# Kernel optimization log

Measured on AMD Instinct MI355X. Metric: run time of the kernel, lower is better.

Reference implementation:

```python
import jax, jax.numpy as jnp
import numpy as np

# BatchNorm1d in eval mode with default init (gamma=1, beta=0, mean=0, var=1):
# y = x / sqrt(1 + eps)
BN_S = 1.0 / float(np.sqrt(1.0 + 1e-5))
ROI_THRESH = 0.8
DN = ('NCHW', 'OIHW', 'NCHW')


def conv(x, w, stride=1, pad=1):
    return jax.lax.conv_general_dilated(x, w, (stride, stride), ((pad, pad), (pad, pad)), dimension_numbers=DN)


def inv_conv(x, w):
    # dense equivalent of spconv.SparseInverseConv2d paired with a stride-2, pad-1, k=3 conv:
    # adjoint index map = transposed conv (lhs_dilation=2, flipped kernel, pad (1,2))
    return jax.lax.conv_general_dilated(x, jnp.flip(w, (2, 3)), (1, 1), ((1, 2), (1, 2)), lhs_dilation=(2, 2), dimension_numbers=DN)


def downsample_mask(m):
    # active-site generation rule of a stride-2, pad-1, k=3 sparse conv == 3x3/stride-2 max pool
    return jax.lax.reduce_window(m, 0.0, jax.lax.max, (1, 1, 3, 3), (1, 1, 2, 2), ((0, 0), (0, 0), (1, 1), (1, 1)))


def setup_inputs():
    key = jax.random.key(0)
    ks = jax.random.split(key, 24)
    b, n_i, H, W = 2, 4, 384, 384
    s = 0.1  # weight scale to keep activations bounded through the conv stack
    inp = {
        'x': jax.random.normal(ks[0], (b, 64, H // 4, W // 4), jnp.float32),
        'image': jax.random.normal(ks[1], (b, 3, H, W), jnp.float32),
        'masks': jax.random.uniform(ks[2], (b, n_i, H, W), jnp.float32),
        'roi_masks': jax.random.uniform(ks[3], (b, n_i, H, W), jnp.float32),
        'w1a': jax.random.normal(ks[4], (32, 4, 3, 3), jnp.float32) * s,
        'w1b': jax.random.normal(ks[5], (32, 32, 3, 3), jnp.float32) * s,
        'w2a': jax.random.normal(ks[6], (32, 32, 3, 3), jnp.float32) * s,
        'w2b': jax.random.normal(ks[7], (32, 32, 3, 3), jnp.float32) * s,
        'w4a': jax.random.normal(ks[8], (64, 32, 3, 3), jnp.float32) * s,
        'w4b': jax.random.normal(ks[9], (64, 64, 3, 3), jnp.float32) * s,
        'inv4_w': jax.random.normal(ks[10], (64, 64, 3, 3), jnp.float32) * s,
        'l4_sub_w': jax.random.normal(ks[11], (32, 64, 3, 3), jnp.float32) * s,
        'inv2_w': jax.random.normal(ks[12], (32, 32, 3, 3), jnp.float32) * s,
        'l5_sub_w': jax.random.normal(ks[13], (32, 32, 3, 3), jnp.float32) * s,
        'r4_w1': jax.random.normal(ks[14], (32, 64, 3, 3), jnp.float32) * s,
        'r4_w2': jax.random.normal(ks[15], (1, 32, 3, 3), jnp.float32) * s,
        'r4_b2': jax.random.normal(ks[16], (1,), jnp.float32) * s,
        'r1_w1': jax.random.normal(ks[17], (32, 32, 3, 3), jnp.float32) * s,
        'r1_w2': jax.random.normal(ks[18], (1, 32, 3, 3), jnp.float32) * s,
        'r1_b2': jax.random.normal(ks[19], (1,), jnp.float32) * s,
    }
    return inp


def reference(x, image, masks, roi_masks, w1a, w1b, w2a, w2b, w4a, w4b, inv4_w, l4_sub_w, inv2_w, l5_sub_w, r4_w1, r4_w2, r4_b2, r1_w1, r1_w2, r1_b2):
    # Faithful dense emulation of predict_details: SubMConv == conv(masked x)*mask,
    # stride-2 SparseConv == conv(masked x) masked by max-pooled mask,
    # SparseInverseConv == transposed conv masked by parent-resolution mask,
    # Fsp.sparse_add on shared indices == masked add, dense()-99/+99 == where(mask, v, -99).
    b, n_i, H, W = masks.shape
    N = b * n_i
    m = masks.reshape(N, 1, H, W)
    roi = roi_masks.reshape(N, 1, H, W)
    img = jnp.broadcast_to(image[:, None], (b, n_i, 3, H, W)).reshape(N, 3, H, W)
    inp = jnp.concatenate([img, m], axis=1)  # [N,4,H,W]

    mask1 = (roi > ROI_THRESH).astype(inp.dtype)
    mask2 = downsample_mask(mask1)
    mask4 = downsample_mask(mask2)

    # low_os1_module: SubMConv, ReLU, BN, SubMConv, ReLU, BN
    f = jnp.maximum(conv(inp * mask1, w1a) * mask1, 0.0) * BN_S
    fea1 = jnp.maximum(conv(f, w1b) * mask1, 0.0) * BN_S  # [N,32,H,W]
    # low_os2_module: stride-2 SparseConv, ReLU, BN, SubMConv, ReLU, BN
    g = jnp.maximum(conv(fea1, w2a, stride=2) * mask2, 0.0) * BN_S
    fea2 = jnp.maximum(conv(g, w2b) * mask2, 0.0) * BN_S  # [N,32,H/2,W/2]
    # low_os4_module
    h = jnp.maximum(conv(fea2, w4a, stride=2) * mask4, 0.0) * BN_S
    fea3 = jnp.maximum(conv(h, w4b) * mask4, 0.0) * BN_S  # [N,64,H/4,W/4]

    # gather dense OS4 features at sparse sites (batch index // n_i) + sparse_add
    xg = jnp.broadcast_to(x[:, None], (b, n_i) + x.shape[1:]).reshape(N, *x.shape[1:]) * mask4
    xs = xg + fea3

    # refine_OS4: SubMConv, BN, leaky, SubMConv(+bias); dense() with -99 off-support
    t = jax.nn.leaky_relu(conv(xs, r4_w1) * mask4 * BN_S, 0.2)
    t = (conv(t, r4_w2) + r4_b2[None, :, None, None]) * mask4
    x_os4_out = jnp.where(mask4 > 0, t, -99.0)

    # layer4: SparseInverseConv(64->64) to OS2 sites, BN, leaky, SubMConv(64->32); add fea2
    u = jax.nn.leaky_relu(inv_conv(xs, inv4_w) * mask2 * BN_S, 0.2)
    u = conv(u, l4_sub_w) * mask2 + fea2
    # layer5: SparseInverseConv(32->32) to OS1 sites, BN, leaky, SubMConv(32->32); add fea1
    v = jax.nn.leaky_relu(inv_conv(u, inv2_w) * mask1 * BN_S, 0.2)
    v = conv(v, l5_sub_w) * mask1 + fea1

    # refine_OS1
    t1 = jax.nn.leaky_relu(conv(v, r1_w1) * mask1 * BN_S, 0.2)
    t1 = (conv(t1, r1_w2) + r1_b2[None, :, None, None]) * mask1
    x_os1_out = jnp.where(mask1 > 0, t1, -99.0)
    return x_os4_out, x_os1_out
```

## Files before the change

kernel.cpp:

```cpp
#include <hip/hip_runtime.h>
#include <hip/hip_bf16.h>

using bf16 = __hip_bfloat16;
typedef unsigned char u8;
typedef short bf16x8 __attribute__((ext_vector_type(8)));
typedef short bf16x4 __attribute__((ext_vector_type(4)));
typedef float f32x4 __attribute__((ext_vector_type(4)));

#define BNS 0.9999950000374997f
#define MFMA_B16 __builtin_amdgcn_mfma_f32_16x16x32_bf16

__device__ __forceinline__ short f2bs(float v){ bf16 h = __float2bfloat16(v); return *reinterpret_cast<short*>(&h); }
__device__ __forceinline__ float s2f(short s){ union{unsigned u; float f;} x; x.u = ((unsigned)(unsigned short)s) << 16; return x.f; }
__device__ __forceinline__ float lrelu(float a){ return fmaxf(a, 0.2f*a); }
__device__ __forceinline__ bf16x8 ld8(const short* p){ return *(const bf16x8*)(p); }


__global__ __launch_bounds__(256) void k_mask1(const float* __restrict__ roi, u8* __restrict__ m1, int total){
    int i = blockIdx.x*256 + threadIdx.x;
    if (i < total) m1[i] = (roi[i] > 0.8f) ? 1 : 0;
}

__global__ __launch_bounds__(256) void k_down(const u8* __restrict__ mi, u8* __restrict__ mo,
                                              int IH, int IW, int OH, int OW){
    int p = blockIdx.x*256 + threadIdx.x;
    int n = blockIdx.y;
    if (p >= OH*OW) return;
    int oy = p / OW, ox = p - oy*OW;
    const u8* src = mi + (size_t)n*IH*IW;
    int v = 0;
    #pragma unroll
    for (int ky=0; ky<3; ky++){
        int iy = 2*oy + ky - 1;
        if ((unsigned)iy >= (unsigned)IH) continue;
        #pragma unroll
        for (int kx=0; kx<3; kx++){
            int ix = 2*ox + kx - 1;
            if ((unsigned)ix < (unsigned)IW) v |= src[iy*IW + ix];
        }
    }
    mo[(size_t)n*OH*OW + p] = (u8)v;
}

__global__ __launch_bounds__(256) void k_wprep(const float* __restrict__ w1b,
                                               const float* __restrict__ i2,
                                               const float* __restrict__ l5,
                                               const float* __restrict__ r1a,
                                               const float* __restrict__ w2b,
                                               const float* __restrict__ w2a,
                                               short* __restrict__ dst){
    int a = blockIdx.y;
    const float* src = (a==0)? w1b : (a==1)? i2 : (a==2)? l5 : (a==3)? r1a : (a==4)? w2b : w2a;
    float sc = (a==2) ? 1.0f : BNS;
    int j = blockIdx.x*256 + threadIdx.x;
    if (j < 9216){
        int co = j/288, r = j%288, ci = r/9, k = r%9;
        dst[a*9216 + k*1024 + co*32 + ci] = f2bs(src[j]*sc);
    }
}

__global__ __launch_bounds__(256) void k_wprep4(const float* __restrict__ inv4,
                                                const float* __restrict__ w4b,
                                                const float* __restrict__ l4s,
                                                const float* __restrict__ r4w1,
                                                const float* __restrict__ w4a,
                                                short* __restrict__ dst)
{
    int a = blockIdx.y;
// ... 87 lines not shown
        for (int g=0; g<G; ++g) acc[u2][g] = (f32x4){0,0,0,0};

    #pragma unroll
    for (int h=0; h<HV; ++h){
        const short* bh[U2N];
        #pragma unroll
        for (int u2=0; u2<U2N; ++u2){
            int ty = u2*4 + wv;
            bh[u2] = s_in + (h*4+nQ)*PS + (ty*18 + nn)*8;
        }
        #pragma unroll
        for (int ky=0; ky<3; ++ky)
            #pragma unroll
            for (int kx=0; kx<3; ++kx){
                const int k = ky*3+kx;
                bf16x8 a[G];
                #pragma unroll
                for (int g=0; g<G; ++g)
                    a[g] = *(const bf16x8*)(wT + k*COUT*CIN + (g*16+nn)*CIN + h*32 + nQ*8);
                #pragma unroll
                for (int u2=0; u2<U2N; ++u2){
                    bf16x8 bfr = ld8(bh[u2] + (ky*18+kx)*8);
                    #pragma unroll
                    for (int g=0; g<G; ++g)
                        acc[u2][g] = MFMA_B16(a[g], bfr, acc[u2][g], 0,0,0);
                }
            }
    }

    #pragma unroll
    for (int u2=0; u2<U2N; ++u2){
        int nt = u2*4 + wv;
        int p = (y0+nt)*H + x0+nn;
        u8 m = s_m[nt*16 + nn];
        short* op = out + ((size_t)n*HW + p)*COUT;
        #pragma unroll
        for (int g=0; g<G; ++g){
            float r[4];
            #pragma unroll
            for (int e=0; e<4; ++e){
                int co = g*16 + nQ*4 + e;
                float a = acc[u2][g][e], o;
                if      (EPI == 0) o = m ? fmaxf(a,0.f) : 0.f;
                else if (EPI == 1) o = m ? lrelu(a) : 0.f;
                else o = m ? fmaxf(a,0.f) + res32[((size_t)(n>>2)*COUT + co)*(size_t)HW + p] : 0.f;
                r[e] = o;
            }
            bf16x4 w4 = {f2bs(r[0]),f2bs(r[1]),f2bs(r[2]),f2bs(r[3])};
            *(bf16x4*)(op + g*16 + nQ*4) = w4;
        }
    }
}

template<int TH>
__global__ __launch_bounds__(256) void mconv_head32(const short* __restrict__ in, int H,
                                                    const short* __restrict__ wTh,
                                                    const float* __restrict__ bias,
                                                    const u8* __restrict__ mask,
                                                    float* __restrict__ out, int tilesX)
{
    const int HW = H*H;
    const int SR = TH + 2, SITES = SR*18;
    const int PS = (SITES|1)*8;
    int tY = blockIdx.x / tilesX, tX = blockIdx.x % tilesX, n = blockIdx.z;
    int y0 = tY*TH, x0 = tX*16;

    __shared__ __align__(16) short s_in[4*((SITES|1)*8)];
    __shared__ u8 s_m[TH*16];

    int tid = threadIdx.x;
    const short* inN = in + (size_t)n*HW*32;
    for (int i = tid; i < SITES*4; i += 256){
        int r = i>>2, q = i&3;
        int ry = r/18, rx = r%18;
        int gy = y0-1+ry, gx = x0-1+rx;
        bf16x8 v = {0,0,0,0,0,0,0,0};
        if ((unsigned)gy < (unsigned)H && (unsigned)gx < (unsigned)H)
            v = *(const bf16x8*)(inN + ((size_t)gy*H + gx)*32 + q*8);
        *(bf16x8*)(s_in + q*PS + r*8) = v;
    }
    for (int i = tid; i < TH*16; i += 256){
        int ty = i>>4, tx = i&15;
        s_m[i] = mask[(size_t)n*HW + (y0+ty)*H + x0+tx];
    }
    __syncthreads();

    int wv = tid >> 6, lane = tid & 63;
    int nQ = lane >> 4, nn = lane & 15;
    float bb = bias[0];

    for (int nt = wv; nt < TH; nt += 4){
        const short* bp = s_in + nQ*PS + (nt*18 + nn)*8;
        f32x4 acc = {0,0,0,0};
        #pragma unroll
        for (int ky=0; ky<3; ++ky)
            #pragma unroll
            for (int kx=0; kx<3; ++kx){
                const int k = ky*3+kx;
                bf16x8 aw = *(const bf16x8*)(wTh + k*512 + nn*32 + nQ*8);
                bf16x8 bfr = ld8(bp + (ky*18+kx)*8);
                acc = MFMA_B16(aw, bfr, acc, 0,0,0);
            }
        if (nQ == 0){
            u8 m = s_m[nt*16 + nn];
            int p = (y0+nt)*H + x0+nn;
            out[(size_t)n*HW + p] = m ? acc[0] + bb : -99.f;
        }
    }
}

template<int COUT, int THO>
__global__ __launch_bounds__(256) void mconv_s2m(const short* __restrict__ in, int IH,
                                                 const short* __restrict__ wT,
                                                 const u8* __restrict__ mask,
                                                 short* __restrict__ out, int OH, int tilesX)
{
    const int IHW = IH*IH, OHW = OH*OH, G = COUT/16;
    const int IR = 2*THO + 1;
    const int SITES = IR*33;
    const int PS = (SITES|1)*8;
    const int ITN = THO/4;
    int tY = blockIdx.x / tilesX, tX = blockIdx.x % tilesX, n = blockIdx.z;
    int y0 = tY*THO, x0 = tX*16;

    __shared__ __align__(16) short s_in[4*((SITES|1)*8)];
    __shared__ u8 s_m[THO*16];

    int tid = threadIdx.x;
    const short* inN = in + (size_t)n*IHW*32;
    for (int i = tid; i < SITES*4; i += 256){
        int r = i>>2, q = i&3;
        int ry = r/33, rx = r%33;
        int gy = 2*y0-1+ry, gx = 2*x0-1+rx;
        bf16x8 v = {0,0,0,0,0,0,0,0};
        if ((unsigned)gy < (unsigned)IH && (unsigned)gx < (unsigned)IH)
            v = *(const bf16x8*)(inN + ((size_t)gy*IH + gx)*32 + q*8);
        *(bf16x8*)(s_in + q*PS + r*8) = v;
    }
    for (int i = tid; i < THO*16; i += 256){
        int ty = i>>4, tx = i&15;
        s_m[i] = mask[(size_t)n*OHW + (y0+ty)*OH + x0+tx];
    }
    __syncthreads();

    int wv = tid >> 6, lane = tid & 63;
    int nQ = lane >> 4, nn = lane & 15;

    f32x4 acc[ITN][G];
    #pragma unroll
    for (int it=0; it<ITN; ++it)
        #pragma unroll
        for (int g=0; g<G; ++g) acc[it][g] = (f32x4){0,0,0,0};

    const short* pb[ITN];
    #pragma unroll
    for (int it=0; it<ITN; ++it){
        int nt = it*4 + wv;
        pb[it] = s_in + nQ*PS + ((2*nt)*33 + 2*nn)*8;
    }

    #pragma unroll
    for (int ky=0; ky<3; ++ky)
        #pragma unroll
        for (int kx=0; kx<3; ++kx){
            const int k = ky*3+kx;
            bf16x8 a[G];
            #pragma unroll
            for (int g=0; g<G; ++g)
                a[g] = *(const bf16x8*)(wT + k*COUT*32 + (g*16+nn)*32 + nQ*8);
            #pragma unroll
            for (int it=0; it<ITN; ++it){
                bf16x8 bfr = ld8(pb[it] + (ky*33+kx)*8);
                #pragma unroll
                for (int g=0; g<G; ++g)
                    acc[it][g] = MFMA_B16(a[g], bfr, acc[it][g], 0,0,0);
            }
        }

    #pragma unroll
    for (int it=0; it<ITN; ++it){
        int nt = it*4 + wv;
        int p = (y0+nt)*OH + x0+nn;
        u8 m = s_m[nt*16 + nn];
        short* op = out + ((size_t)n*OHW + p)*COUT;
        #pragma unroll
        for (int g=0; g<G; ++g){
            float r[4];
            #pragma unroll
            for (int e=0; e<4; ++e) r[e] = m ? fmaxf(acc[it][g][e],0.f) : 0.f;
            bf16x4 w4 = {f2bs(r[0]),f2bs(r[1]),f2bs(r[2]),f2bs(r[3])};
            *(bf16x4*)(op + g*16 + nQ*4) = w4;
        }
    }
}

__global__ __launch_bounds__(256) void conv1ab3(const float* __restrict__ image,
                                                const float* __restrict__ masks,
                                                const u8*  __restrict__ M1,
                                                const short* __restrict__ wT1a,
                                                const short* __restrict__ wT1b,
                                                short* __restrict__ fea1)
{
    const int H = 384; const int HW = H*H;
    const int PS = 181*8;
    int tY = blockIdx.x / 48, tX = blockIdx.x % 48, n = blockIdx.z;
    int y0 = tY*16, x0 = tX*8;

    __shared__ float s_inp[4][240];
    __shared__ u8    s_m[240];
    __shared__ int   s_cnt[2];
    __shared__ unsigned short s_lF[180];
    __shared__ unsigned short s_lO[128];
    __shared__ __align__(16) short s_ic[8*(181*8)];
    __shared__ __align__(16) short s_f[4*(181*8)];

    int tid = threadIdx.x;
    const bf16x8 Z8 = {0,0,0,0,0,0,0,0};
    if (tid < 2) s_cnt[tid] = 0;
    for (int i = tid; i < 4*181; i += 256)
        *(bf16x8*)(s_f + i*8) = Z8;
    for (int i = tid; i < 240; i += 256){
        int ly = i/12, lxx = i%12;
        int gy = y0-2+ly, gx = x0-2+lxx;
        bool inb = ((unsigned)gy < 384u) && ((unsigned)gx < 384u);
        u8 mv = inb ? M1[(size_t)n*HW + gy*H + gx] : 0;
        s_m[i] = mv;
        float mm = (float)mv;
        int p = gy*H + gx;
        #pragma unroll
        for (int c = 0; c < 4; ++c){
            float v = 0.f;
            if (inb) v = (c < 3) ? image[((size_t)(n>>2)*3 + c)*HW + p]
                                 : masks[(size_t)n*HW + p];
            s_inp[c][i] = v*mm;
        }
    }
    __syncthreads();

    for (int i = tid; i < 180; i += 256){
        int fy = i/10, fx = i - fy*10;
        if (s_m[(fy+1)*12 + fx+1]){
            int idx = atomicAdd(&s_cnt[0], 1);
            s_lF[idx] = (unsigned short)i;
        }
    }
    for (int i = tid; i < 128; i += 256){
        int ty = i>>3, tx = i&7;
        if (s_m[(ty+2)*12 + tx+2]){
            int idx = atomicAdd(&s_cnt[1], 1);
            s_lO[idx] = (unsigned short)i;
        }
    }
    __syncthreads();

    int cntF = s_cnt[0], cntO = s_cnt[1];

    {
        int q = tid & 63;
        int ci = q/9, kk = q - ci*9, ky = kk/3, kx = kk - ky*3;
        bool qok = q < 36;
        for (int i = tid; i < cntF*64; i += 256){
            int site = s_lF[i >> 6];
            short v = 0;
            if (qok){
                int fy = site/10, fx = site - fy*10;
                v = f2bs(s_inp[ci][(fy+ky)*12 + fx+kx]);
            }
            s_ic[(q>>3)*PS + site*8 + (q&7)] = v;
        }
    }
    __syncthreads();

    int wv = tid >> 6, lane = tid & 63;
    int nQ = lane >> 4, nn = lane & 15;

    {
        bf16x8 fa0[2], fa1[2];
        #pragma unroll
        for (int h=0;h<2;++h){
            fa0[h] = *(const bf16x8*)(wT1a + h*1024 + nn*32 + nQ*8);
            fa1[h] = *(const bf16x8*)(wT1a + h*1024 + (16+nn)*32 + nQ*8);
        }
        for (int base = wv*16; base < cntF; base += 64){
            int slot = base + nn;
            bool on = slot < cntF;
            int site = s_lF[on ? slot : 0];
            f32x4 a0 = {0,0,0,0}, a1 = {0,0,0,0};
            #pragma unroll
            for (int h=0;h<2;++h){
                bf16x8 bfr = ld8(s_ic + (h*4+nQ)*PS + site*8);
                a0 = MFMA_B16(fa0[h], bfr, a0, 0,0,0);
                a1 = MFMA_B16(fa1[h], bfr, a1, 0,0,0);
            }
            if (on){
                #pragma unroll
                for (int g=0; g<2; ++g){
                    float r[4];
                    #pragma unroll
                    for (int e=0; e<4; ++e){
                        float a = g ? a1[e] : a0[e];
                        r[e] = fmaxf(a,0.f);
                    }
                    bf16x4 w4 = {f2bs(r[0]),f2bs(r[1]),f2bs(r[2]),f2bs(r[3])};
                    *(bf16x4*)(s_f + (g*2 + (nQ>>1))*PS + site*8 + (nQ&1)*4) = w4;
                }
            }
        }
    }
    __syncthreads();

    {
        for (int base = wv*16; base < cntO; base += 64){
            int slot = base + nn;
            bool on = slot < cntO;
            int os = s_lO[on ? slot : 0];
            int ty = os >> 3, tx = os & 7;
            const short* pb = s_f + nQ*PS + (ty*10 + tx)*8;
            f32x4 acc0 = {0,0,0,0}, acc1 = {0,0,0,0};
            #pragma unroll
            for (int ky=0; ky<3; ++ky)
                #pragma unroll
                for (int kx=0; kx<3; ++kx){
                    const int k = ky*3+kx;
                    bf16x8 a0 = *(const bf16x8*)(wT1b + k*1024 + nn*32 + nQ*8);
                    bf16x8 a1 = *(const bf16x8*)(wT1b + k*1024 + (16+nn)*32 + nQ*8);
                    bf16x8 bfr = ld8(pb + (ky*10+kx)*8);
                    acc0 = MFMA_B16(a0, bfr, acc0, 0,0,0);
                    acc1 = MFMA_B16(a1, bfr, acc1, 0,0,0);
                }
// ... 163 lines not shown
                }
            }
        #pragma unroll
        for (int u2 = 0; u2 < 4; ++u2){
            int nt = u2*4 + wv;
            int p = (y0+nt)*H2 + x0+nn;
            u8 m = s_m[(nt+1)*18 + nn+1];
            short* up = u_out + ((size_t)n*HW2 + p)*32;
            #pragma unroll
            for (int g=0; g<2; ++g){
                float r[4];
                #pragma unroll
                for (int e=0; e<4; ++e){
                    float a = g ? acc1[u2][e] : acc0[u2][e];
                    r[e] = m ? a + s2f(pf2v[u2][g][e]) : 0.f;
                }
                bf16x4 w4 = {f2bs(r[0]),f2bs(r[1]),f2bs(r[2]),f2bs(r[3])};
                *(bf16x4*)(up + g*16 + nQ*4) = w4;
            }
        }
    }
}

__global__ __launch_bounds__(256) void fk_back8(const short* __restrict__ u,
                                                const short* __restrict__ fea1,
                                                const u8*  __restrict__ M1,
                                                const short* __restrict__ wTi2,
                                                const short* __restrict__ wTl5,
                                                const short* __restrict__ wTr1a,
                                                const short* __restrict__ wTr1b,
                                                const float* __restrict__ r1_b2,
                                                float* __restrict__ out1)
{
    const int H1 = 384, HW1 = H1*H1, H2 = 192, HW2 = H2*H2;
    const int PS_U = 97*8, PS_A = 309*8, PS_B = 241*8, PS_C = 181*8;
    int tY = blockIdx.x / 48, tX = blockIdx.x % 48, n = blockIdx.z;
    int y0 = tY*16, x0 = tX*8;
    int uy0 = (y0>>1) - 2, ux0 = (x0>>1) - 2;

    __shared__ __align__(16) short sP0[4*(309*8)];
    __shared__ __align__(16) short sP1[4*(241*8)];
    __shared__ u8 s_m[308];
    __shared__ int s_cnt[7];
    __shared__ unsigned s_lA[4*80];
    __shared__ unsigned s_lB[240];
    __shared__ unsigned s_lC[180];
    __shared__ unsigned s_lD[128];
    short* s_u  = sP1;
    short* s_vl = sP0;
    short* s_v  = sP1;
    short* s_t1 = sP0;

    int tid = threadIdx.x;
    const bf16x8 Z8 = {0,0,0,0,0,0,0,0};

    if (tid < 7) s_cnt[tid] = 0;
    const short* uN = u + (size_t)n*HW2*32;
    for (int i = tid; i < 96*4; i += 256){
        int r = i>>2, q = i&3;
        int ly = r >> 3, lxx = r & 7;
        int gy = uy0+ly, gx = ux0+lxx;
        bf16x8 v = Z8;
        if ((unsigned)gy < 192u && (unsigned)gx < 192u)
            v = *(const bf16x8*)(uN + ((size_t)gy*H2 + gx)*32 + q*8);
        *(bf16x8*)(s_u + q*PS_U + r*8) = v;
    }
    for (int i = tid; i < 308; i += 256){
        int ry = i/14, rx = i%14; int gy = y0-3+ry, gx = x0-3+rx;
        s_m[i] = ((unsigned)gy < 384u && (unsigned)gx < 384u) ? M1[(size_t)n*HW1 + gy*H1 + gx] : 0;
    }
    for (int i = tid; i < 4*309; i += 256)
        *(bf16x8*)(s_vl + i*8) = Z8;
    __syncthreads();

    for (int i = tid; i < 308; i += 256){
        if (s_m[i]){
            int ry = i/14, rx = i - ry*14;
            int cls = ((ry&1)<<1) | (rx&1);
            int jr = ry>>1, jc = rx>>1;
            int idx = atomicAdd(&s_cnt[cls], 1);
            s_lA[cls*80 + idx] = ((unsigned)i<<16) | (unsigned)(jr*8+jc);
        }
    }
    for (int i = tid; i < 240; i += 256){
        int vy = i/12, vx = i - vy*12;
        if (s_m[(vy+1)*14 + vx+1]){
            int idx = atomicAdd(&s_cnt[4], 1);
            s_lB[idx] = ((unsigned)i<<16) | (unsigned)(vy*14+vx);
        }
    }
    for (int i = tid; i < 180; i += 256){
        int qy = i/10, qx = i - qy*10;
        if (s_m[(qy+2)*14 + qx+2]){
            int idx = atomicAdd(&s_cnt[5], 1);
            s_lC[idx] = ((unsigned)i<<16) | (unsigned)(qy*12+qx);
        }
    }
    for (int i = tid; i < 128; i += 256){
        int ty = i>>3, tx = i&7;
        if (s_m[(ty+3)*14 + tx+3]){
            int idx = atomicAdd(&s_cnt[6], 1);
            s_lD[idx] = ((unsigned)i<<16) | (unsigned)(ty*10+tx);
        } else {
            out1[(size_t)n*HW1 + (size_t)(y0+ty)*H1 + (x0+tx)] = -99.f;
        }
    }
    __syncthreads();

    int wv = tid >> 6, lane = tid & 63;
    int nQ = lane >> 4, nn = lane & 15;

    {
        const int tN_[4]   = {4,2,2,1};
        const int tOff[4][4] = {{0,1,8,9},{1,9,9,9},{8,9,9,9},{9,9,9,9}};
        const int tWk [4][4] = {{8,6,2,0},{7,1,1,1},{5,3,3,3},{4,4,4,4}};
        int cnt = s_cnt[wv];
        int tn = tN_[wv];
        for (int base = 0; base < cnt; base += 16){
            int slot = base + nn;
            bool on = slot < cnt;
            unsigned e = s_lA[wv*80 + (on ? slot : 0)];
            int rb = e & 0xffff;
            f32x4 acc0 = {0,0,0,0}, acc1 = {0,0,0,0};
            for (int t = 0; t < tn; ++t){
                bf16x8 bfr = ld8(s_u + nQ*PS_U + (rb + tOff[wv][t])*8);
                const short* wp = wTi2 + tWk[wv][t]*1024;
                bf16x8 a0 = *(const bf16x8*)(wp + nn*32 + nQ*8);
                bf16x8 a1 = *(const bf16x8*)(wp + (16+nn)*32 + nQ*8);
                acc0 = MFMA_B16(a0, bfr, acc0, 0,0,0);
                acc1 = MFMA_B16(a1, bfr, acc1, 0,0,0);
            }
            if (on){
                int sidx = e >> 16;
                float r[8];
                #pragma unroll
                for (int g=0; g<2; ++g)
                    #pragma unroll
                    for (int ee=0; ee<4; ++ee)
                        r[g*4+ee] = lrelu(g ? acc1[ee] : acc0[ee]);
                bf16x4 w0 = {f2bs(r[0]),f2bs(r[1]),f2bs(r[2]),f2bs(r[3])};
                bf16x4 w1 = {f2bs(r[4]),f2bs(r[5]),f2bs(r[6]),f2bs(r[7])};
                *(bf16x4*)(s_vl + (nQ>>1)*PS_A     + sidx*8 + (nQ&1)*4) = w0;
                *(bf16x4*)(s_vl + (2+(nQ>>1))*PS_A + sidx*8 + (nQ&1)*4) = w1;
            }
        }
    }
    __syncthreads();

    for (int i = tid; i < 4*241; i += 256)
        *(bf16x8*)(s_v + i*8) = Z8;
    __syncthreads();

    {
        int cnt = s_cnt[4];
        for (int base = wv*16; base < cnt; base += 64){
            int slot = base + nn;
            bool on = slot < cnt;
            unsigned e = s_lB[on ? slot : 0];
            int rb = e & 0xffff;
            int wr = e >> 16;
            int vy = wr/12, vx = wr - vy*12;
            const short* f1 = fea1 + ((size_t)n*HW1 + (size_t)(y0-2+vy)*H1 + (x0-2+vx))*32;
            bf16x4 p0 = *(const bf16x4*)(f1 + nQ*4);
            bf16x4 p1 = *(const bf16x4*)(f1 + 16 + nQ*4);
            const short* pv = s_vl + nQ*PS_A + rb*8;
            f32x4 acc0 = {0,0,0,0}, acc1 = {0,0,0,0};
            #pragma unroll
            for (int ky=0; ky<3; ++ky)
                #pragma unroll
                for (int kx=0; kx<3; ++kx){
                    const int k = ky*3+kx;
                    bf16x8 wb0 = *(const bf16x8*)(wTl5 + k*1024 + nn*32 + nQ*8);
                    bf16x8 wb1 = *(const bf16x8*)(wTl5 + k*1024 + (16+nn)*32 + nQ*8);
                    bf16x8 bfr = ld8(pv + (ky*14+kx)*8);
                    acc0 = MFMA_B16(wb0, bfr, acc0, 0,0,0);
                    acc1 = MFMA_B16(wb1, bfr, acc1, 0,0,0);
                }
            if (on){
                float r[8];
                #pragma unroll
                for (int ee=0; ee<4; ++ee){
                    r[ee]   = acc0[ee] + s2f(p0[ee]);
                    r[4+ee] = acc1[ee] + s2f(p1[ee]);
                }
                bf16x4 w0 = {f2bs(r[0]),f2bs(r[1]),f2bs(r[2]),f2bs(r[3])};
                bf16x4 w1 = {f2bs(r[4]),f2bs(r[5]),f2bs(r[6]),f2bs(r[7])};
                *(bf16x4*)(s_v + (nQ>>1)*PS_B     + wr*8 + (nQ&1)*4) = w0;
                *(bf16x4*)(s_v + (2+(nQ>>1))*PS_B + wr*8 + (nQ&1)*4) = w1;
            }
        }
    }
    __syncthreads();

    for (int i = tid; i < 4*181; i += 256)
        *(bf16x8*)(s_t1 + i*8) = Z8;
    __syncthreads();

    {
        int cnt = s_cnt[5];
        for (int base = wv*16; base < cnt; base += 64){
            int slot = base + nn;
            bool on = slot < cnt;
            unsigned e = s_lC[on ? slot : 0];
            int rb = e & 0xffff;
            const short* pv = s_v + nQ*PS_B + rb*8;
            f32x4 acc0 = {0,0,0,0}, acc1 = {0,0,0,0};
            #pragma unroll
            for (int ky=0; ky<3; ++ky)
                #pragma unroll
                for (int kx=0; kx<3; ++kx){
                    const int k = ky*3+kx;
                    bf16x8 wc0 = *(const bf16x8*)(wTr1a + k*1024 + nn*32 + nQ*8);
                    bf16x8 wc1 = *(const bf16x8*)(wTr1a + k*1024 + (16+nn)*32 + nQ*8);
                    bf16x8 bfr = ld8(pv + (ky*12+kx)*8);
                    acc0 = MFMA_B16(wc0, bfr, acc0, 0,0,0);
                    acc1 = MFMA_B16(wc1, bfr, acc1, 0,0,0);
                }
            if (on){
                int wr = e >> 16;
                float r[8];
                #pragma unroll
                for (int g=0; g<2; ++g)
                    #pragma unroll
                    for (int ee=0; ee<4; ++ee)
                        r[g*4+ee] = lrelu(g ? acc1[ee] : acc0[ee]);
                bf16x4 w0 = {f2bs(r[0]),f2bs(r[1]),f2bs(r[2]),f2bs(r[3])};
                bf16x4 w1 = {f2bs(r[4]),f2bs(r[5]),f2bs(r[6]),f2bs(r[7])};
                *(bf16x4*)(s_t1 + (nQ>>1)*PS_C     + wr*8 + (nQ&1)*4) = w0;
                *(bf16x4*)(s_t1 + (2+(nQ>>1))*PS_C + wr*8 + (nQ&1)*4) = w1;
            }
        }
    }
    __syncthreads();

    {
        float bb = r1_b2[0];
        int cnt = s_cnt[6];
        for (int base = wv*16; base < cnt; base += 64){
            int slot = base + nn;
            bool on = slot < cnt;
            unsigned e = s_lD[on ? slot : 0];
            int rb = e & 0xffff;
            const short* pt = s_t1 + nQ*PS_C + rb*8;
            f32x4 acc = {0,0,0,0};
            #pragma unroll
            for (int ky=0; ky<3; ++ky)
                #pragma unroll
                for (int kx=0; kx<3; ++kx){
                    const int k = ky*3+kx;
                    bf16x8 aw = *(const bf16x8*)(wTr1b + k*512 + nn*32 + nQ*8);
                    bf16x8 bfr = ld8(pt + (ky*10+kx)*8);
// ... 40 lines not shown
    const int H2 = 192, HW2 = 192*192;
    const int H4 = 96,  HW4 = 96*96;

    char* wsp = (char*)d_ws;
    size_t off = 0;
    auto alloc = [&](size_t bytes) -> char* {
        char* p = wsp + off;
        off += (bytes + 255) & ~(size_t)255;
        return p;
    };
    bf16* FEA1 = (bf16*)alloc((size_t)N*32*HW1*2);
    u8*   M1   = (u8*)alloc((size_t)N*HW1);
    u8*   M2   = (u8*)alloc((size_t)N*HW2);
    u8*   M4   = (u8*)alloc((size_t)N*HW4);
    bf16* FEA2 = (bf16*)alloc((size_t)N*32*HW2*2);
    bf16* XS   = (bf16*)alloc((size_t)N*64*HW4*2);
    bf16* GU   = (bf16*)alloc((size_t)N*32*HW2*2);
    bf16* HT   = (bf16*)alloc((size_t)N*64*HW4*2);
    short* WT   = (short*)alloc(6*9216*2);
    short* WT4  = (short*)alloc((size_t)129024*2);
    short* WT1a = (short*)alloc(2048*2);
    short* WTh  = (short*)alloc(2*4608*2);
    (void)ws_size; (void)in_sizes; (void)n_in; (void)out_size;

    short* wT1b  = WT;
    short* wTi2  = WT + 9216;
    short* wTl5  = WT + 2*9216;
    short* wTr1a = WT + 3*9216;
    short* wT2b  = WT + 4*9216;
    short* wT2a  = WT + 5*9216;
    short* wTi4  = WT4;
    short* wT4b  = WT4 + 36864;
    short* wTl4  = WT4 + 73728;
    short* wTr4a = WT4 + 92160;
    short* wT4a  = WT4 + 110592;
    short* wTr1b = WTh;
    short* wTr4b = WTh + 4608;

    dim3 blk(256);

    k_mask1<<<dim3((N*HW1 + 255)/256), blk, 0, stream>>>(roi, M1, N*HW1);
    k_down<<<dim3((HW2 + 255)/256, N), blk, 0, stream>>>(M1, M2, H1, H1, H2, H2);
    k_down<<<dim3((HW4 + 255)/256, N), blk, 0, stream>>>(M2, M4, H2, H2, H4, H4);
    k_wprep<<<dim3(36, 6), blk, 0, stream>>>(w1b, inv2_w, l5_sub, r1_w1, w2b, w2a, WT);
    k_wprep4<<<dim3(144, 5), blk, 0, stream>>>(inv4_w, w4b, l4_sub, r4_w1, w4a, WT4);
    k_wprep_misc<<<dim3(18, 3), blk, 0, stream>>>(w1a, r1_w2, r4_w2, WT1a, WTh);

    conv1ab3<<<dim3(1152, 1, N), blk, 0, stream>>>(image, masks, M1, WT1a, wT1b, (short*)FEA1);
    mconv_s2m<32,8><<<dim3(288, 1, N), blk, 0, stream>>>((const short*)FEA1, H1, wT2a, M2, (short*)GU, H2, 12);
    mconv_s1<32,32,0,8><<<dim3(288, 1, N), blk, 0, stream>>>((const short*)GU, H2, wT2b, M2, nullptr, (short*)FEA2, 12);
    mconv_s2m<64,4><<<dim3(144, 1, N), blk, 0, stream>>>((const short*)FEA2, H2, wT4a, M4, (short*)HT, H4, 6);
    mconv_s1<64,64,3,4><<<dim3(144, 1, N), blk, 0, stream>>>((const short*)HT, H4, wT4b, M4, x, (short*)XS, 6);

    mconv_s1<64,32,1,4><<<dim3(144, 1, N), blk, 0, stream>>>((const short*)XS, H4, wTr4a, M4, nullptr, (short*)HT, 6);
    mconv_head32<4><<<dim3(144, 1, N), blk, 0, stream>>>((const short*)HT, H4, wTr4b, r4_b2, M4, out, 6);

    fk_l4c<<<dim3(144, 1, N), blk, 0, stream>>>((const short*)XS, (const short*)FEA2, M2,
                                                wTi4, wTl4, (short*)GU);

    fk_back8<<<dim3(1152, 1, N), blk, 0, stream>>>((const short*)GU, (const short*)FEA1, M1,
                                                   wTi2, wTl5, wTr1a, wTr1b, r1_b2,
                                                   out + (size_t)N*HW4);
}
```

Baseline: 528.4 us.

## Fuse refine_OS4 convs into one kernel; ballot-compact site lists; zero only inactive sites

Merges the refine_OS4 64->32 conv and the 32->1 head into a single kernel that keeps the intermediate in shared memory with a halo, removing one launch and a global round trip. The halo sites are recomputed by neighbouring tiles. Active-site list building in conv1ab3 and fk_back8 now uses wave ballots with one atomic per wave instead of one per site. Shared buffers are zeroed only at inactive sites instead of everywhere, which also removes several barriers.

```diff
diff --git a/kernel.cpp b/kernel.cpp
--- a/kernel.cpp
+++ b/kernel.cpp
@@ -14,6 +14,9 @@
 __device__ __forceinline__ float s2f(short s){ union{unsigned u; float f;} x; x.u = ((unsigned)(unsigned short)s) << 16; return x.f; }
 __device__ __forceinline__ float lrelu(float a){ return fmaxf(a, 0.2f*a); }
 __device__ __forceinline__ bf16x8 ld8(const short* p){ return *(const bf16x8*)(p); }
+__device__ __forceinline__ int lane_prefix(unsigned long long b){
+    return __builtin_amdgcn_mbcnt_hi((unsigned)(b>>32), __builtin_amdgcn_mbcnt_lo((unsigned)b, 0u));
+}
 
 
 __global__ __launch_bounds__(256) void k_mask1(const float* __restrict__ roi, u8* __restrict__ m1, int total){
@@ -207,63 +210,6 @@
     }
 }
 
-template<int TH>
-__global__ __launch_bounds__(256) void mconv_head32(const short* __restrict__ in, int H,
-                                                    const short* __restrict__ wTh,
-                                                    const float* __restrict__ bias,
-                                                    const u8* __restrict__ mask,
-                                                    float* __restrict__ out, int tilesX)
-{
-    const int HW = H*H;
-    const int SR = TH + 2, SITES = SR*18;
-    const int PS = (SITES|1)*8;
-    int tY = blockIdx.x / tilesX, tX = blockIdx.x % tilesX, n = blockIdx.z;
-    int y0 = tY*TH, x0 = tX*16;
-
-    __shared__ __align__(16) short s_in[4*((SITES|1)*8)];
-    __shared__ u8 s_m[TH*16];
-
-    int tid = threadIdx.x;
-    const short* inN = in + (size_t)n*HW*32;
-    for (int i = tid; i < SITES*4; i += 256){
-        int r = i>>2, q = i&3;
-        int ry = r/18, rx = r%18;
-        int gy = y0-1+ry, gx = x0-1+rx;
-        bf16x8 v = {0,0,0,0,0,0,0,0};
-        if ((unsigned)gy < (unsigned)H && (unsigned)gx < (unsigned)H)
-            v = *(const bf16x8*)(inN + ((size_t)gy*H + gx)*32 + q*8);
-        *(bf16x8*)(s_in + q*PS + r*8) = v;
-    }
-    for (int i = tid; i < TH*16; i += 256){
-        int ty = i>>4, tx = i&15;
-        s_m[i] = mask[(size_t)n*HW + (y0+ty)*H + x0+tx];
-    }
-    __syncthreads();
-
-    int wv = tid >> 6, lane = tid & 63;
-    int nQ = lane >> 4, nn = lane & 15;
-    float bb = bias[0];
-
-    for (int nt = wv; nt < TH; nt += 4){
-        const short* bp = s_in + nQ*PS + (nt*18 + nn)*8;
-        f32x4 acc = {0,0,0,0};
-        #pragma unroll
-        for (int ky=0; ky<3; ++ky)
-            #pragma unroll
-            for (int kx=0; kx<3; ++kx){
-                const int k = ky*3+kx;
-                bf16x8 aw = *(const bf16x8*)(wTh + k*512 + nn*32 + nQ*8);
-                bf16x8 bfr = ld8(bp + (ky*18+kx)*8);
-                acc = MFMA_B16(aw, bfr, acc, 0,0,0);
-            }
-        if (nQ == 0){
-            u8 m = s_m[nt*16 + nn];
-            int p = (y0+nt)*H + x0+nn;
-            out[(size_t)n*HW + p] = m ? acc[0] + bb : -99.f;
-        }
-    }
-}
-
 template<int COUT, int THO>
 __global__ __launch_bounds__(256) void mconv_s2m(const short* __restrict__ in, int IH,
                                                  const short* __restrict__ wT,
@@ -349,6 +295,108 @@
     }
 }
 
+template<int TH>
+__global__ __launch_bounds__(256) void mconv_ref4(const short* __restrict__ in, int H,
+                                                  const short* __restrict__ wTa,
+                                                  const short* __restrict__ wTh,
+                                                  const float* __restrict__ bias,
+                                                  const u8* __restrict__ mask,
+                                                  float* __restrict__ out, int tilesX)
+{
+    const int HW = H*H;
+    const int XR = TH+4, XSITES = XR*20;
+    const int PSX = (XSITES|1)*8;
+    const int TR = TH+2, TSITES = TR*18;
+    const int PST = (TSITES|1)*8;
+    int tY = blockIdx.x / tilesX, tX = blockIdx.x % tilesX, n = blockIdx.z;
+    int y0 = tY*TH, x0 = tX*16;
+
+    __shared__ __align__(16) short s_xs[8*((XSITES|1)*8)];
+    __shared__ __align__(16) short s_t[4*((TSITES|1)*8)];
+    __shared__ u8 s_m[TSITES];
+
+    int tid = threadIdx.x;
+    const short* inN = in + (size_t)n*HW*64;
+    for (int i = tid; i < XSITES*8; i += 256){
+        int r = i>>3, q = i&7;
+        int ry = r/20, rx = r%20;
+        int gy = y0-2+ry, gx = x0-2+rx;
+        bf16x8 v = {0,0,0,0,0,0,0,0};
+        if ((unsigned)gy < (unsigned)H && (unsigned)gx < (unsigned)H)
+            v = *(const bf16x8*)(inN + ((size_t)gy*H + gx)*64 + q*8);
+        *(bf16x8*)(s_xs + q*PSX + r*8) = v;
+    }
+    for (int i = tid; i < TSITES; i += 256){
+        int vy = i/18, vx = i%18;
+        int gy = y0-1+vy, gx = x0-1+vx;
+        s_m[i] = ((unsigned)gy < (unsigned)H && (unsigned)gx < (unsigned)H) ? mask[(size_t)n*HW + gy*H + gx] : 0;
+    }
+    __syncthreads();
+
+    int wv = tid >> 6, lane = tid & 63;
+    int nQ = lane >> 4, nn = lane & 15;
+
+    const int TG = (TSITES + 15)/16;
+    for (int g8 = wv; g8 < TG; g8 += 4){
+        int s0 = g8*16 + nn;
+        int s = s0 >= TSITES ? TSITES-1 : s0;
+        int vy = s/18, vx = s - vy*18;
+        const short* pb = s_xs + nQ*PSX + (vy*20 + vx)*8;
+        f32x4 acc0 = {0,0,0,0}, acc1 = {0,0,0,0};
+        #pragma unroll
+        for (int ky=0; ky<3; ++ky)
+            #pragma unroll
+            for (int kx=0; kx<3; ++kx){
+                const int k = ky*3+kx;
+                const short* wk = wTa + k*2048;
+                bf16x8 xlo = ld8(pb + (ky*20+kx)*8);
+                bf16x8 xhi = ld8(pb + 4*PSX + (ky*20+kx)*8);
+                bf16x8 a0lo = *(const bf16x8*)(wk + nn*64 + nQ*8);
+                bf16x8 a0hi = *(const bf16x8*)(wk + nn*64 + 32 + nQ*8);
+                bf16x8 a1lo = *(const bf16x8*)(wk + (16+nn)*64 + nQ*8);
+                bf16x8 a1hi = *(const bf16x8*)(wk + (16+nn)*64 + 32 + nQ*8);
+                acc0 = MFMA_B16(a0lo, xlo, acc0, 0,0,0);
+                acc0 = MFMA_B16(a0hi, xhi, acc0, 0,0,0);
+                acc1 = MFMA_B16(a1lo, xlo, acc1, 0,0,0);
+                acc1 = MFMA_B16(a1hi, xhi, acc1, 0,0,0);
+            }
+        if (s0 < TSITES){
+            u8 m = s_m[s0];
+            #pragma unroll
+            for (int g=0; g<2; ++g){
+                float r[4];
+                #pragma unroll
+                for (int e=0; e<4; ++e){
+                    float a = g ? acc1[e] : acc0[e];
+                    r[e] = m ? lrelu(a) : 0.f;
+                }
+                bf16x4 w4 = {f2bs(r[0]),f2bs(r[1]),f2bs(r[2]),f2bs(r[3])};
+                *(bf16x4*)(s_t + (g*2 + (nQ>>1))*PST + s0*8 + (nQ&1)*4) = w4;
+            }
+        }
+    }
+    __syncthreads();
+
+    float bb = bias[0];
+    for (int nt = wv; nt < TH; nt += 4){
+        const short* pt = s_t + nQ*PST + (nt*18 + nn)*8;
+        f32x4 acc = {0,0,0,0};
+        #pragma unroll
+        for (int ky=0; ky<3; ++ky)
+            #pragma unroll
+            for (int kx=0; kx<3; ++kx){
+                const int k = ky*3+kx;
+                bf16x8 aw = *(const bf16x8*)(wTh + k*512 + nn*32 + nQ*8);
+                bf16x8 bfr = ld8(pt + (ky*18+kx)*8);
+                acc = MFMA_B16(aw, bfr, acc, 0,0,0);
+            }
+        if (nQ == 0){
+            u8 m = s_m[(nt+1)*18 + nn+1];
+            out[(size_t)n*HW + (size_t)(y0+nt)*H + (x0+nn)] = m ? acc[0] + bb : -99.f;
+        }
+    }
+}
+
 __global__ __launch_bounds__(256) void conv1ab3(const float* __restrict__ image,
                                                 const float* __restrict__ masks,
                                                 const u8*  __restrict__ M1,
@@ -370,10 +418,9 @@
     __shared__ __align__(16) short s_f[4*(181*8)];
 
     int tid = threadIdx.x;
+    int wv = tid >> 6, lane = tid & 63;
     const bf16x8 Z8 = {0,0,0,0,0,0,0,0};
     if (tid < 2) s_cnt[tid] = 0;
-    for (int i = tid; i < 4*181; i += 256)
-        *(bf16x8*)(s_f + i*8) = Z8;
     for (int i = tid; i < 240; i += 256){
         int ly = i/12, lxx = i%12;
         int gy = y0-2+ly, gx = x0-2+lxx;
@@ -392,18 +439,32 @@
     }
     __syncthreads();
 
-    for (int i = tid; i < 180; i += 256){
-        int fy = i/10, fx = i - fy*10;
-        if (s_m[(fy+1)*12 + fx+1]){
-            int idx = atomicAdd(&s_cnt[0], 1);
-            s_lF[idx] = (unsigned short)i;
-        }
-    }
-    for (int i = tid; i < 128; i += 256){
-        int ty = i>>3, tx = i&7;
-        if (s_m[(ty+2)*12 + tx+2]){
-            int idx = atomicAdd(&s_cnt[1], 1);
-            s_lO[idx] = (unsigned short)i;
+    for (int base = wv*64; base < 180; base += 256){
+        int i = base + lane;
+        bool act = false;
+        if (i < 180){ int fy = i/10, fx = i - fy*10; act = s_m[(fy+1)*12 + fx+1] != 0; }
+        unsigned long long bal = __ballot(act);
+        int tot = __popcll(bal);
+        if (tot){
+            int pre = lane_prefix(bal);
+            int wb;
+            if (lane == 0) wb = atomicAdd(&s_cnt[0], tot);
+            wb = __shfl(wb, 0);
+            if (act) s_lF[wb + pre] = (unsigned short)i;
+        }
+    }
+    for (int base = wv*64; base < 128; base += 256){
+        int i = base + lane;
+        bool act = false;
+        if (i < 128){ int ty = i>>3, tx = i&7; act = s_m[(ty+2)*12 + tx+2] != 0; }
+        unsigned long long bal = __ballot(act);
+        int tot = __popcll(bal);
+        if (tot){
+            int pre = lane_prefix(bal);
+            int wb;
+            if (lane == 0) wb = atomicAdd(&s_cnt[1], tot);
+            wb = __shfl(wb, 0);
+            if (act) s_lO[wb + pre] = (unsigned short)i;
         }
     }
     __syncthreads();
@@ -426,10 +487,14 @@
     }
     __syncthreads();
 
-    int wv = tid >> 6, lane = tid & 63;
     int nQ = lane >> 4, nn = lane & 15;
 
     {
+        for (int i = tid; i < 180*4; i += 256){
+            int site = i >> 2, q = i & 3;
+            int fy = site/10, fx = site - fy*10;
+            if (!s_m[(fy+1)*12 + fx+1]) *(bf16x8*)(s_f + q*PS + site*8) = Z8;
+        }
         bf16x8 fa0[2], fa1[2];
         #pragma unroll
         for (int h=0;h<2;++h){
@@ -699,6 +764,7 @@
     short* s_t1 = sP0;
 
     int tid = threadIdx.x;
+    int wv = tid >> 6, lane = tid & 63;
     const bf16x8 Z8 = {0,0,0,0,0,0,0,0};
 
     if (tid < 7) s_cnt[tid] = 0;
@@ -716,48 +782,93 @@
         int ry = i/14, rx = i%14; int gy = y0-3+ry, gx = x0-3+rx;
         s_m[i] = ((unsigned)gy < 384u && (unsigned)gx < 384u) ? M1[(size_t)n*HW1 + gy*H1 + gx] : 0;
     }
-    for (int i = tid; i < 4*309; i += 256)
-        *(bf16x8*)(s_vl + i*8) = Z8;
-    __syncthreads();
-
-    for (int i = tid; i < 308; i += 256){
-        if (s_m[i]){
+    __syncthreads();
+
+    for (int base = wv*64; base < 308; base += 256){
+        int i = base + lane;
+        int cls = -1; unsigned pack = 0;
+        if (i < 308 && s_m[i]){
             int ry = i/14, rx = i - ry*14;
-            int cls = ((ry&1)<<1) | (rx&1);
-            int jr = ry>>1, jc = rx>>1;
-            int idx = atomicAdd(&s_cnt[cls], 1);
-            s_lA[cls*80 + idx] = ((unsigned)i<<16) | (unsigned)(jr*8+jc);
-        }
-    }
-    for (int i = tid; i < 240; i += 256){
-        int vy = i/12, vx = i - vy*12;
-        if (s_m[(vy+1)*14 + vx+1]){
-            int idx = atomicAdd(&s_cnt[4], 1);
-            s_lB[idx] = ((unsigned)i<<16) | (unsigned)(vy*14+vx);
-        }
-    }
-    for (int i = tid; i < 180; i += 256){
-        int qy = i/10, qx = i - qy*10;
-        if (s_m[(qy+2)*14 + qx+2]){
-            int idx = atomicAdd(&s_cnt[5], 1);
-            s_lC[idx] = ((unsigned)i<<16) | (unsigned)(qy*12+qx);
-        }
-    }
-    for (int i = tid; i < 128; i += 256){
-        int ty = i>>3, tx = i&7;
-        if (s_m[(ty+3)*14 + tx+3]){
-            int idx = atomicAdd(&s_cnt[6], 1);
-            s_lD[idx] = ((unsigned)i<<16) | (unsigned)(ty*10+tx);
-        } else {
-            out1[(size_t)n*HW1 + (size_t)(y0+ty)*H1 + (x0+tx)] = -99.f;
-        }
-    }
-    __syncthreads();
-
-    int wv = tid >> 6, lane = tid & 63;
+            cls = ((ry&1)<<1) | (rx&1);
+            pack = ((unsigned)i<<16) | (unsigned)((ry>>1)*8 + (rx>>1));
+        }
+        #pragma unroll
+        for (int c = 0; c < 4; ++c){
+            unsigned long long bal = __ballot(cls == c);
+            int tot = __popcll(bal);
+            if (tot){
+                int pre = lane_prefix(bal);
+                int wb;
+                if (lane == 0) wb = atomicAdd(&s_cnt[c], tot);
+                wb = __shfl(wb, 0);
+                if (cls == c) s_lA[c*80 + wb + pre] = pack;
+            }
+        }
+    }
+    for (int base = wv*64; base < 240; base += 256){
+        int i = base + lane;
+        bool act = false; unsigned pack = 0;
+        if (i < 240){
+            int vy = i/12, vx = i - vy*12;
+            act = s_m[(vy+1)*14 + vx+1] != 0;
+            pack = ((unsigned)i<<16) | (unsigned)(vy*14 + vx);
+        }
+        unsigned long long bal = __ballot(act);
+        int tot = __popcll(bal);
+        if (tot){
+            int pre = lane_prefix(bal);
+            int wb;
+            if (lane == 0) wb = atomicAdd(&s_cnt[4], tot);
+            wb = __shfl(wb, 0);
+            if (act) s_lB[wb + pre] = pack;
+        }
+    }
+    for (int base = wv*64; base < 180; base += 256){
+        int i = base + lane;
+        bool act = false; unsigned pack = 0;
+        if (i < 180){
+            int qy = i/10, qx = i - qy*10;
+            act = s_m[(qy+2)*14 + qx+2] != 0;
+            pack = ((unsigned)i<<16) | (unsigned)(qy*12 + qx);
+        }
+        unsigned long long bal = __ballot(act);
+        int tot = __popcll(bal);
+        if (tot){
+            int pre = lane_prefix(bal);
+            int wb;
+            if (lane == 0) wb = atomicAdd(&s_cnt[5], tot);
+            wb = __shfl(wb, 0);
+            if (act) s_lC[wb + pre] = pack;
+        }
+    }
+    for (int base = wv*64; base < 128; base += 256){
+        int i = base + lane;
+        bool act = false; unsigned pack = 0;
+        if (i < 128){
+            int ty = i>>3, tx = i&7;
+            act = s_m[(ty+3)*14 + tx+3] != 0;
+            pack = ((unsigned)i<<16) | (unsigned)(ty*10 + tx);
+            if (!act) out1[(size_t)n*HW1 + (size_t)(y0+ty)*H1 + (x0+tx)] = -99.f;
+        }
+        unsigned long long bal = __ballot(act);
+        int tot = __popcll(bal);
+        if (tot){
+            int pre = lane_prefix(bal);
+            int wb;
+            if (lane == 0) wb = atomicAdd(&s_cnt[6], tot);
+            wb = __shfl(wb, 0);
+            if (act) s_lD[wb + pre] = pack;
+        }
+    }
+    __syncthreads();
+
     int nQ = lane >> 4, nn = lane & 15;
 
     {
+        for (int i = tid; i < 308*4; i += 256){
+            int site = i >> 2, q = i & 3;
+            if (!s_m[site]) *(bf16x8*)(s_vl + q*PS_A + site*8) = Z8;
+        }
         const int tN_[4]   = {4,2,2,1};
         const int tOff[4][4] = {{0,1,8,9},{1,9,9,9},{8,9,9,9},{9,9,9,9}};
         const int tWk [4][4] = {{8,6,2,0},{7,1,1,1},{5,3,3,3},{4,4,4,4}};
@@ -794,11 +905,12 @@
     }
     __syncthreads();
 
-    for (int i = tid; i < 4*241; i += 256)
-        *(bf16x8*)(s_v + i*8) = Z8;
-    __syncthreads();
-
     {
+        for (int i = tid; i < 240*4; i += 256){
+            int site = i >> 2, q = i & 3;
+            int vy = site/12, vx = site - vy*12;
+            if (!s_m[(vy+1)*14 + vx+1]) *(bf16x8*)(s_v + q*PS_B + site*8) = Z8;
+        }
         int cnt = s_cnt[4];
         for (int base = wv*16; base < cnt; base += 64){
             int slot = base + nn;
@@ -839,11 +951,12 @@
     }
     __syncthreads();
 
-    for (int i = tid; i < 4*181; i += 256)
-        *(bf16x8*)(s_t1 + i*8) = Z8;
-    __syncthreads();
-
     {
+        for (int i = tid; i < 180*4; i += 256){
+            int site = i >> 2, q = i & 3;
+            int qy = site/10, qx = site - qy*10;
+            if (!s_m[(qy+2)*14 + qx+2]) *(bf16x8*)(s_t1 + q*PS_C + site*8) = Z8;
+        }
         int cnt = s_cnt[5];
         for (int base = wv*16; base < cnt; base += 64){
             int slot = base + nn;
@@ -990,8 +1103,7 @@
     mconv_s2m<64,4><<<dim3(144, 1, N), blk, 0, stream>>>((const short*)FEA2, H2, wT4a, M4, (short*)HT, H4, 6);
     mconv_s1<64,64,3,4><<<dim3(144, 1, N), blk, 0, stream>>>((const short*)HT, H4, wT4b, M4, x, (short*)XS, 6);
 
-    mconv_s1<64,32,1,4><<<dim3(144, 1, N), blk, 0, stream>>>((const short*)XS, H4, wTr4a, M4, nullptr, (short*)HT, 6);
-    mconv_head32<4><<<dim3(144, 1, N), blk, 0, stream>>>((const short*)HT, H4, wTr4b, r4_b2, M4, out, 6);
+    mconv_ref4<4><<<dim3(144, 1, N), blk, 0, stream>>>((const short*)XS, H4, wTr4a, wTr4b, r4_b2, M4, out, 6);
 
     fk_l4c<<<dim3(144, 1, N), blk, 0, stream>>>((const short*)XS, (const short*)FEA2, M2,
                                                 wTi4, wTl4, (short*)GU);
```

Result: slower. 542.9 us (+2.7%).

## Fuse refine_OS4 two-conv chain into one kernel with halo recompute

Applied to the files above, without the earlier changes.

Merges the refine_OS4 first SubMConv (64->32, lrelu) and the head conv (32->1 with bias and -99 fill) into a single kernel. The intermediate activation stays in shared memory, computed over a 1-pixel halo from a 2-pixel-halo input tile, so it is never written to or read back from global memory and one launch is dropped. The cost is redundant halo computation and larger shared memory per block, which may lower occupancy. These are small OS4 kernels, so the overall effect is modest.

```diff
diff --git a/kernel.cpp b/kernel.cpp
--- a/kernel.cpp
+++ b/kernel.cpp
@@ -207,63 +207,6 @@
     }
 }
 
-template<int TH>
-__global__ __launch_bounds__(256) void mconv_head32(const short* __restrict__ in, int H,
-                                                    const short* __restrict__ wTh,
-                                                    const float* __restrict__ bias,
-                                                    const u8* __restrict__ mask,
-                                                    float* __restrict__ out, int tilesX)
-{
-    const int HW = H*H;
-    const int SR = TH + 2, SITES = SR*18;
-    const int PS = (SITES|1)*8;
-    int tY = blockIdx.x / tilesX, tX = blockIdx.x % tilesX, n = blockIdx.z;
-    int y0 = tY*TH, x0 = tX*16;
-
-    __shared__ __align__(16) short s_in[4*((SITES|1)*8)];
-    __shared__ u8 s_m[TH*16];
-
-    int tid = threadIdx.x;
-    const short* inN = in + (size_t)n*HW*32;
-    for (int i = tid; i < SITES*4; i += 256){
-        int r = i>>2, q = i&3;
-        int ry = r/18, rx = r%18;
-        int gy = y0-1+ry, gx = x0-1+rx;
-        bf16x8 v = {0,0,0,0,0,0,0,0};
-        if ((unsigned)gy < (unsigned)H && (unsigned)gx < (unsigned)H)
-            v = *(const bf16x8*)(inN + ((size_t)gy*H + gx)*32 + q*8);
-        *(bf16x8*)(s_in + q*PS + r*8) = v;
-    }
-    for (int i = tid; i < TH*16; i += 256){
-        int ty = i>>4, tx = i&15;
-        s_m[i] = mask[(size_t)n*HW + (y0+ty)*H + x0+tx];
-    }
-    __syncthreads();
-
-    int wv = tid >> 6, lane = tid & 63;
-    int nQ = lane >> 4, nn = lane & 15;
-    float bb = bias[0];
-
-    for (int nt = wv; nt < TH; nt += 4){
-        const short* bp = s_in + nQ*PS + (nt*18 + nn)*8;
-        f32x4 acc = {0,0,0,0};
-        #pragma unroll
-        for (int ky=0; ky<3; ++ky)
-            #pragma unroll
-            for (int kx=0; kx<3; ++kx){
-                const int k = ky*3+kx;
-                bf16x8 aw = *(const bf16x8*)(wTh + k*512 + nn*32 + nQ*8);
-                bf16x8 bfr = ld8(bp + (ky*18+kx)*8);
-                acc = MFMA_B16(aw, bfr, acc, 0,0,0);
-            }
-        if (nQ == 0){
-            u8 m = s_m[nt*16 + nn];
-            int p = (y0+nt)*H + x0+nn;
-            out[(size_t)n*HW + p] = m ? acc[0] + bb : -99.f;
-        }
-    }
-}
-
 template<int COUT, int THO>
 __global__ __launch_bounds__(256) void mconv_s2m(const short* __restrict__ in, int IH,
                                                  const short* __restrict__ wT,
@@ -345,6 +288,108 @@
             for (int e=0; e<4; ++e) r[e] = m ? fmaxf(acc[it][g][e],0.f) : 0.f;
             bf16x4 w4 = {f2bs(r[0]),f2bs(r[1]),f2bs(r[2]),f2bs(r[3])};
             *(bf16x4*)(op + g*16 + nQ*4) = w4;
+        }
+    }
+}
+
+template<int TH>
+__global__ __launch_bounds__(256) void mconv_ref4(const short* __restrict__ in, int H,
+                                                  const short* __restrict__ wTa,
+                                                  const short* __restrict__ wTh,
+                                                  const float* __restrict__ bias,
+                                                  const u8* __restrict__ mask,
+                                                  float* __restrict__ out, int tilesX)
+{
+    const int HW = H*H;
+    const int XR = TH+4, XSITES = XR*20;
+    const int PSX = (XSITES|1)*8;
+    const int TR = TH+2, TSITES = TR*18;
+    const int PST = (TSITES|1)*8;
+    int tY = blockIdx.x / tilesX, tX = blockIdx.x % tilesX, n = blockIdx.z;
+    int y0 = tY*TH, x0 = tX*16;
+
+    __shared__ __align__(16) short s_xs[8*((XSITES|1)*8)];
+    __shared__ __align__(16) short s_t[4*((TSITES|1)*8)];
+    __shared__ u8 s_m[TSITES];
+
+    int tid = threadIdx.x;
+    const short* inN = in + (size_t)n*HW*64;
+    for (int i = tid; i < XSITES*8; i += 256){
+        int r = i>>3, q = i&7;
+        int ry = r/20, rx = r%20;
+        int gy = y0-2+ry, gx = x0-2+rx;
+        bf16x8 v = {0,0,0,0,0,0,0,0};
+        if ((unsigned)gy < (unsigned)H && (unsigned)gx < (unsigned)H)
+            v = *(const bf16x8*)(inN + ((size_t)gy*H + gx)*64 + q*8);
+        *(bf16x8*)(s_xs + q*PSX + r*8) = v;
+    }
+    for (int i = tid; i < TSITES; i += 256){
+        int vy = i/18, vx = i%18;
+        int gy = y0-1+vy, gx = x0-1+vx;
+        s_m[i] = ((unsigned)gy < (unsigned)H && (unsigned)gx < (unsigned)H) ? mask[(size_t)n*HW + gy*H + gx] : 0;
+    }
+    __syncthreads();
+
+    int wv = tid >> 6, lane = tid & 63;
+    int nQ = lane >> 4, nn = lane & 15;
+
+    const int TG = (TSITES + 15)/16;
+    for (int g8 = wv; g8 < TG; g8 += 4){
+        int s0 = g8*16 + nn;
+        int s = s0 >= TSITES ? TSITES-1 : s0;
+        int vy = s/18, vx = s - vy*18;
+        const short* pb = s_xs + nQ*PSX + (vy*20 + vx)*8;
+        f32x4 acc0 = {0,0,0,0}, acc1 = {0,0,0,0};
+        #pragma unroll
+        for (int ky=0; ky<3; ++ky)
+            #pragma unroll
+            for (int kx=0; kx<3; ++kx){
+                const int k = ky*3+kx;
+                const short* wk = wTa + k*2048;
+                bf16x8 xlo = ld8(pb + (ky*20+kx)*8);
+                bf16x8 xhi = ld8(pb + 4*PSX + (ky*20+kx)*8);
+                bf16x8 a0lo = *(const bf16x8*)(wk + nn*64 + nQ*8);
+                bf16x8 a0hi = *(const bf16x8*)(wk + nn*64 + 32 + nQ*8);
+                bf16x8 a1lo = *(const bf16x8*)(wk + (16+nn)*64 + nQ*8);
+                bf16x8 a1hi = *(const bf16x8*)(wk + (16+nn)*64 + 32 + nQ*8);
+                acc0 = MFMA_B16(a0lo, xlo, acc0, 0,0,0);
+                acc0 = MFMA_B16(a0hi, xhi, acc0, 0,0,0);
+                acc1 = MFMA_B16(a1lo, xlo, acc1, 0,0,0);
+                acc1 = MFMA_B16(a1hi, xhi, acc1, 0,0,0);
+            }
+        if (s0 < TSITES){
+            u8 m = s_m[s0];
+            #pragma unroll
+            for (int g=0; g<2; ++g){
+                float r[4];
+                #pragma unroll
+                for (int e=0; e<4; ++e){
+                    float a = g ? acc1[e] : acc0[e];
+                    r[e] = m ? lrelu(a) : 0.f;
+                }
+                bf16x4 w4 = {f2bs(r[0]),f2bs(r[1]),f2bs(r[2]),f2bs(r[3])};
+                *(bf16x4*)(s_t + (g*2 + (nQ>>1))*PST + s0*8 + (nQ&1)*4) = w4;
+            }
+        }
+    }
+    __syncthreads();
+
+    float bb = bias[0];
+    for (int nt = wv; nt < TH; nt += 4){
+        const short* pt = s_t + nQ*PST + (nt*18 + nn)*8;
+        f32x4 acc = {0,0,0,0};
+        #pragma unroll
+        for (int ky=0; ky<3; ++ky)
+            #pragma unroll
+            for (int kx=0; kx<3; ++kx){
+                const int k = ky*3+kx;
+                bf16x8 aw = *(const bf16x8*)(wTh + k*512 + nn*32 + nQ*8);
+                bf16x8 bfr = ld8(pt + (ky*18+kx)*8);
+                acc = MFMA_B16(aw, bfr, acc, 0,0,0);
+            }
+        if (nQ == 0){
+            u8 m = s_m[(nt+1)*18 + nn+1];
+            out[(size_t)n*HW + (size_t)(y0+nt)*H + (x0+nn)] = m ? acc[0] + bb : -99.f;
         }
     }
 }
@@ -990,8 +1035,7 @@
     mconv_s2m<64,4><<<dim3(144, 1, N), blk, 0, stream>>>((const short*)FEA2, H2, wT4a, M4, (short*)HT, H4, 6);
     mconv_s1<64,64,3,4><<<dim3(144, 1, N), blk, 0, stream>>>((const short*)HT, H4, wT4b, M4, x, (short*)XS, 6);
 
-    mconv_s1<64,32,1,4><<<dim3(144, 1, N), blk, 0, stream>>>((const short*)XS, H4, wTr4a, M4, nullptr, (short*)HT, 6);
-    mconv_head32<4><<<dim3(144, 1, N), blk, 0, stream>>>((const short*)HT, H4, wTr4b, r4_b2, M4, out, 6);
+    mconv_ref4<4><<<dim3(144, 1, N), blk, 0, stream>>>((const short*)XS, H4, wTr4a, wTr4b, r4_b2, M4, out, 6);
 
     fk_l4c<<<dim3(144, 1, N), blk, 0, stream>>>((const short*)XS, (const short*)FEA2, M2,
                                                 wTi4, wTl4, (short*)GU);
```

After: 521.6 us. No clear change (-1.3%).
